# Optimization experiments

Measured on AMD Instinct MI355X. Metric: run time of the kernel, lower is better.

Reference implementation:

```python
import jax, jax.numpy as jnp
import numpy as np

NUM_CLASSES = 4
TOPK = 300            # k = min(300, A); A = 75600 >> 300
BETA = 0.1            # SmoothL1 beta
SMOOTH = 0.05         # cls label smoothing
BOX_W, OBJ_W, CLS_W = 2.0, 1.0, 1.0


def setup_inputs() -> dict:
    key = jax.random.key(0)
    k1, k2, k3 = jax.random.split(key, 3)
    predictions = jax.random.normal(k1, (32, 25200, 27), dtype=jnp.float32)
    targets_box = jax.random.uniform(k2, (32, 50, 4), dtype=jnp.float32)
    targets_cls = jax.random.randint(k3, (32, 50), 0, NUM_CLASSES, dtype=jnp.int32)
    return {"predictions": predictions, "targets_box": targets_box, "targets_cls": targets_cls}


def _xywh_to_xyxy(b):
    half_w = b[:, 2] * 0.5
    half_h = b[:, 3] * 0.5
    return jnp.stack([b[:, 0] - half_w, b[:, 1] - half_h,
                      b[:, 0] + half_w, b[:, 1] + half_h], axis=1)


def _pairwise_iou_xywh(boxes1, boxes2):
    # boxes1: [N,4], boxes2: [M,4] -> [N,M]
    b1 = _xywh_to_xyxy(boxes1)[:, None, :]   # [N,1,4]
    b2 = _xywh_to_xyxy(boxes2)[None, :, :]   # [1,M,4]
    inter_w = jnp.clip(jnp.minimum(b1[..., 2], b2[..., 2]) - jnp.maximum(b1[..., 0], b2[..., 0]), 0)
    inter_h = jnp.clip(jnp.minimum(b1[..., 3], b2[..., 3]) - jnp.maximum(b1[..., 1], b2[..., 1]), 0)
    inter = inter_w * inter_h
    area1 = (b1[..., 2] - b1[..., 0]) * (b1[..., 3] - b1[..., 1])
    area2 = (b2[..., 2] - b2[..., 0]) * (b2[..., 3] - b2[..., 1])
    union = area1 + area2 - inter
    return jnp.where(union > 0, inter / union, 0.0)


def _bce_logits(x, y):
    # BCEWithLogits: softplus(x) - x*y (numerically stable)
    return jax.nn.softplus(x) - x * y


def _smooth_l1(x, y):
    d = jnp.abs(x - y)
    return jnp.where(d < BETA, 0.5 * d * d / BETA, d - 0.5 * BETA)


def _per_sample(pred, tbox, tcls):
    # pred: [anchors, 27] -> all_anchors: [A, 9]
    nf = 5 + NUM_CLASSES
    all_anchors = pred.reshape(-1, nf)
    A = all_anchors.shape[0]
    box_logits = all_anchors[:, :4]
    obj_logits = all_anchors[:, 4]
    cls_logits = all_anchors[:, 5:5 + NUM_CLASSES]
    box_preds = jax.nn.sigmoid(box_logits)

    tcls = jnp.clip(tcls.astype(jnp.int32), 0, NUM_CLASSES - 1)   # [T]
    tboxes = jnp.clip(tbox, 0.0, 1.0)                              # [T,4]

    k = min(TOPK, A)
    _, topk_idx = jax.lax.top_k(obj_logits, k)                     # [k]
    p_boxes_k = box_preds[topk_idx]                                # [k,4]
    ious = _pairwise_iou_xywh(p_boxes_k, tboxes)                   # [k,T]
    best_idx = jnp.argmax(ious, axis=0)                            # [T]
    chosen = topk_idx[best_idx]                                    # [T]

    obj_targets = jnp.zeros((A,), pred.dtype).at[chosen].set(1.0)
    box_targets = jnp.zeros((A, 4), pred.dtype).at[chosen].set(tboxes)
    smooth_pos = 1.0 - SMOOTH
    smooth_neg = SMOOTH / max(NUM_CLASSES - 1, 1)
    cls_targets = jnp.full((A, NUM_CLASSES), smooth_neg, pred.dtype)
    cls_targets = cls_targets.at[chosen, tcls].set(smooth_pos)

    obj_weights = jnp.where(obj_targets > 0, 2.0, 0.5)
    obj_l = jnp.mean(_bce_logits(obj_logits, obj_targets) * obj_weights) * OBJ_W

    pos = (obj_targets > 0).astype(pred.dtype)                     # [A]
    npos = jnp.sum(pos)
    cls_sum = jnp.sum(_bce_logits(cls_logits, cls_targets) * pos[:, None])
    box_sum = jnp.sum(_smooth_l1(box_preds, box_targets) * pos[:, None])
    cls_l = jnp.where(npos > 0, cls_sum / (npos * NUM_CLASSES), 0.0) * CLS_W
    box_l = jnp.where(npos > 0, box_sum / (npos * 4), 0.0) * BOX_W
    return box_l, cls_l, obj_l


def reference(predictions, targets_box, targets_cls):
    box_l, cls_l, obj_l = jax.vmap(_per_sample)(predictions, targets_box, targets_cls)
    box_loss = jnp.sum(box_l)
    cls_loss = jnp.sum(cls_l)
    obj_loss = jnp.sum(obj_l)
    total_loss = box_loss + cls_loss + obj_loss
    return (total_loss, box_loss, cls_loss, obj_loss)
```

## Files before the change

### kernel.cpp

```cpp
#include <hip/hip_runtime.h>
#include <math.h>

#define NBATCH 32
#define AP     75600
#define NF     9
#define KTOP   300
#define NT     50
#define NC     4
#define APB    2048
#define UNR    8
#define NBLKA  37
#define LCAP   256
#define CCAPL  3072
#define MCAP   384
#define EQCAP  1024
#define PREFK  0xC0000000u

__device__ __forceinline__ float sp_f(float x){
    return fmaxf(x, 0.0f) + log1pf(expf(-fabsf(x)));
}
__device__ __forceinline__ float sig_f(float x){
    return 1.0f / (1.0f + expf(-x));
}
__device__ __forceinline__ unsigned fkey(float x){
    unsigned u = __float_as_uint(x);
    return (u & 0x80000000u) ? ~u : (u | 0x80000000u);
}
__device__ __forceinline__ float kinv(unsigned k){
    unsigned u = (k & 0x80000000u) ? (k & 0x7FFFFFFFu) : ~k;
    return __uint_as_float(u);
}


__global__ __launch_bounds__(256) void kA_scan(
    const float* __restrict__ pred, double* __restrict__ partials,
    unsigned* __restrict__ candKey, int* __restrict__ candIdx,
    int* __restrict__ candCnt)
{
    const int s   = blockIdx.y;
    const int blk = blockIdx.x;
    const int tid = threadIdx.x;
    __shared__ unsigned bKey[LCAP];
    __shared__ int      bIdx[LCAP];
    __shared__ int      lcnt;
    __shared__ double   wsum[4];
    if (tid == 0) lcnt = 0;
    __syncthreads();

    const float* p_s = pred + (size_t)s * (AP*NF);
    const int base = blk * APB;

    float o[UNR];
    int   j[UNR];
    bool  ok[UNR];
    #pragma unroll
    for (int u = 0; u < UNR; ++u){
        j[u]  = base + u*256 + tid;
        ok[u] = (j[u] < AP);
        o[u]  = ok[u] ? p_s[(size_t)j[u]*NF + 4] : -1.0f;
    }
    float facc = 0.0f;
    #pragma unroll
    for (int u = 0; u < UNR; ++u){
        if (ok[u]){
            facc += sp_f(o[u]);
            unsigned ky = fkey(o[u]);
            if (ky >= PREFK){
                int p = atomicAdd(&lcnt, 1);
                if (p < LCAP){ bKey[p] = ky; bIdx[p] = j[u]; }
            }
        }
    }
    double acc = (double)facc;
    for (int off = 32; off > 0; off >>= 1) acc += __shfl_down(acc, off);
    if ((tid & 63) == 0) wsum[tid >> 6] = acc;
    __syncthreads();
    if (tid == 0){
        partials[s*NBLKA + blk] = wsum[0] + wsum[1] + wsum[2] + wsum[3];
        candCnt[s*NBLKA + blk] = lcnt;
    }
    const int n = min(lcnt, LCAP);
    unsigned* gk = candKey + ((size_t)s*NBLKA + blk) * LCAP;
    int*      gi = candIdx + ((size_t)s*NBLKA + blk) * LCAP;
    for (int i = tid; i < n; i += 256){ gk[i] = bKey[i]; gi[i] = bIdx[i]; }
}

__device__ __forceinline__ void find_bin_wp(
    const unsigned* hist, int ngroups, unsigned need,
    unsigned* sGS, unsigned* sBin, unsigned* sAbove, int tid)
{
    const int wv = tid >> 6, ln = tid & 63;
    for (int g = wv; g < ngroups; g += 16){
        unsigned v = hist[g*64 + ln];
        #pragma unroll
        for (int off = 32; off > 0; off >>= 1){
            unsigned t = __shfl_down(v, off);
            if (ln + off < 64) v += t;
        }
        if (ln == 0) sGS[g] = v;
    }
    __syncthreads();
    if (wv == 0){
        unsigned gsv = (ln < ngroups) ? sGS[ln] : 0u;
        unsigned inc = gsv;
        #pragma unroll
        for (int off = 1; off < 64; off <<= 1){
            unsigned t = __shfl_down(inc, off);
            if (ln + off < 64) inc += t;
        }
        unsigned excl = inc - gsv;
        bool hit = (ln < ngroups) && (excl < need) && (need <= inc);
        unsigned long long mb = __ballot(hit);
        int gstar = __ffsll(mb) - 1;
        unsigned exG = __shfl(excl, gstar);
        unsigned y = hist[gstar*64 + ln];
        unsigned yinc = y;
        #pragma unroll
        for (int off = 1; off < 64; off <<= 1){
            unsigned t = __shfl_down(yinc, off);
            if (ln + off < 64) yinc += t;
        }
        unsigned above = exG + (yinc - y);
        bool hit2 = (above < need) && (need <= above + y);
        mb = __ballot(hit2);
        int bl = __ffsll(mb) - 1;
        unsigned ab = __shfl(above, bl);
        if (ln == 0){ *sBin = (unsigned)(gstar*64 + bl); *sAbove = ab; }
    }
    __syncthreads();
}

__global__ __launch_bounds__(1024) void kB_finish(
    const float* __restrict__ pred,
    const float* __restrict__ tboxG,
    const int*   __restrict__ tclsG,
    const unsigned* __restrict__ candKeyG, const int* __restrict__ candIdxG,
    const int* __restrict__ candCnt,
    const double* __restrict__ partials,
    float* __restrict__ lossPart)
{
    const int s   = blockIdx.x;
    const int tid = threadIdx.x;
    const int wv  = tid >> 6;
    const int ln  = tid & 63;
    const float* p_s = pred + (size_t)s * (AP*NF);

    __shared__ unsigned cKey[CCAPL];
    __shared__ int      cIdx[CCAPL];
    __shared__ unsigned hist[2048];
    __shared__ unsigned sGS[32];
    __shared__ unsigned sB1, sA1, sB2, sA2, sB3, sA3;
    __shared__ int      bOff[NBLKA + 1];
    __shared__ int      sOk;
    __shared__ int      eqList[EQCAP];
    __shared__ int      eqCnt, mCnt;
    __shared__ unsigned mKey[MCAP];
    __shared__ int      mIdx[MCAP];
    __shared__ float    mB[5][MCAP];
    __shared__ float    tXY[NT][5];
    __shared__ float    tWH[NT][4];
    __shared__ int      tCl[NT];
    __shared__ int      chosenA[NT];
    __shared__ float    corrJ[NT], clsJ[NT], boxJ[NT];
    __shared__ int      lastJ[NT];
    __shared__ double   s_spsum;

    if (tid == 0){ eqCnt = 0; mCnt = 0; }
    if (wv == 0){
        int c  = (ln < NBLKA) ? candCnt[s*NBLKA + ln] : 0;
        int of = (c > LCAP) ? 1 : 0;
        int cc = min(c, LCAP);
        int inc = cc;
        #pragma unroll
        for (int off = 1; off < 64; off <<= 1){
            int t = __shfl_up(inc, off);
            if (ln >= off) inc += t;
        }
        if (ln < NBLKA) bOff[ln + 1] = inc;
        unsigned long long anyof = __ballot(of != 0);
        if (ln == 0) bOff[0] = 0;
        if (ln == NBLKA - 1)
            sOk = (anyof == 0ull && inc >= KTOP && inc <= CCAPL) ? 1 : 0;
    }
    if (wv == 15){
        double a = (ln < NBLKA) ? partials[s*NBLKA + ln] : 0.0;
        for (int off = 32; off > 0; off >>= 1) a += __shfl_down(a, off);
        if (ln == 0) s_spsum = a;
    }
    __syncthreads();
    const bool fast = (sOk != 0);
    const int  n    = fast ? bOff[NBLKA] : 0;

    if (fast){
        for (int b = wv; b < NBLKA; b += 16){
            const int c = min(candCnt[s*NBLKA + b], LCAP);
            const int o = bOff[b];
            const unsigned* gk = candKeyG + ((size_t)s*NBLKA + b) * LCAP;
            const int*      gi = candIdxG + ((size_t)s*NBLKA + b) * LCAP;
            for (int i = ln; i < c; i += 64){ cKey[o+i] = gk[i]; cIdx[o+i] = gi[i]; }
        }
    }
    for (int i = tid; i < 2048; i += 1024) hist[i] = 0;
    __syncthreads();
    if (fast){
        for (int i = tid; i < n; i += 1024) atomicAdd(&hist[cKey[i] >> 21], 1u);
    } else {
        for (int i = tid; i < AP; i += 1024)
            atomicAdd(&hist[fkey(p_s[(size_t)i*NF + 4]) >> 21], 1u);
    }
    __syncthreads();
    find_bin_wp(hist, 32, KTOP, sGS, &sB1, &sA1, tid);
    const unsigned b1 = sB1, ab1 = sA1;
    const unsigned need2 = KTOP - ab1;

    for (int i = tid; i < 2048; i += 1024) hist[i] = 0;
    __syncthreads();
    if (fast){
        for (int i = tid; i < n; i += 1024){
            unsigned ky = cKey[i];
            if ((ky >> 21) == b1) atomicAdd(&hist[(ky >> 10) & 0x7FFu], 1u);
        }
    } else {
        for (int i = tid; i < AP; i += 1024){
            unsigned ky = fkey(p_s[(size_t)i*NF + 4]);
            if ((ky >> 21) == b1) atomicAdd(&hist[(ky >> 10) & 0x7FFu], 1u);
        }
    }
    __syncthreads();
    find_bin_wp(hist, 32, need2, sGS, &sB2, &sA2, tid);
    const unsigned b2 = sB2, ab2 = sA2;
    const unsigned need3 = need2 - ab2;
    const unsigned pref  = (b1 << 11) | b2;

    if (tid < 1024) hist[tid] = 0;
    __syncthreads();
    if (fast){
        for (int i = tid; i < n; i += 1024){
            unsigned ky = cKey[i];
            if ((ky >> 10) == pref) atomicAdd(&hist[ky & 0x3FFu], 1u);
        }
    } else {
        for (int i = tid; i < AP; i += 1024){
            unsigned ky = fkey(p_s[(size_t)i*NF + 4]);
            if ((ky >> 10) == pref) atomicAdd(&hist[ky & 0x3FFu], 1u);
        }
    }
    __syncthreads();
    find_bin_wp(hist, 16, need3, sGS, &sB3, &sA3, tid);
    const unsigned b3 = sB3, ab3 = sA3;
    const unsigned needEq = need3 - ab3;
    const unsigned T = (b1 << 21) | (b2 << 10) | b3;

    if (fast){
        for (int i = tid; i < n; i += 1024){
            if (cKey[i] == T){
                int p = atomicAdd(&eqCnt, 1);
                if (p < EQCAP) eqList[p] = cIdx[i];
            }
        }
    } else {
        for (int i = tid; i < AP; i += 1024){
            if (fkey(p_s[(size_t)i*NF + 4]) == T){
                int p = atomicAdd(&eqCnt, 1);
                if (p < EQCAP) eqList[p] = i;
            }
        }
    }
    __syncthreads();
    const int ne = min(eqCnt, EQCAP);

    const int dom = fast ? n : AP;
    for (int base = wv*64; base < dom; base += 1024){
        int i = base + ln;
        bool mflag = false; unsigned ky = 0; int ix = 0;
        if (i < dom){
            if (fast){ ky = cKey[i]; ix = cIdx[i]; }
            else     { ky = fkey(p_s[(size_t)i*NF + 4]); ix = i; }
            if (ky > T) mflag = true;
            else if (ky == T){
                int r = 0;
                for (int j = 0; j < ne; ++j) r += (eqList[j] < ix) ? 1 : 0;
                mflag = ((unsigned)r < needEq);
            }
        }
        unsigned long long msk = __ballot(mflag);
        int bpos = 0;
        if (ln == 0 && msk) bpos = atomicAdd(&mCnt, (int)__popcll(msk));
        bpos = __shfl(bpos, 0);
        if (mflag){
            int pos = bpos + (int)__popcll(msk & ((1ull << ln) - 1ull));
            if (pos < MCAP){ mKey[pos] = ky; mIdx[pos] = ix; }
        }
    }
    __syncthreads();
    const int kM = min(mCnt, MCAP);

    for (int m = tid; m < kM; m += 1024){
        const float* row = p_s + (size_t)mIdx[m] * NF;
        float bx = sig_f(row[0]), by = sig_f(row[1]);
        float bw = sig_f(row[2]), bh = sig_f(row[3]);
        float hw = bw * 0.5f, hh = bh * 0.5f;
        float x1 = bx - hw, y1 = by - hh, x2 = bx + hw, y2 = by + hh;
        mB[0][m] = x1; mB[1][m] = y1; mB[2][m] = x2; mB[3][m] = y2;
        mB[4][m] = (x2 - x1) * (y2 - y1);
    }
    if (tid >= 512 && tid < 512 + NT){
        int t = tid - 512;
        const float* tb = tboxG + ((size_t)s * NT + t) * 4;
        float cx = fminf(fmaxf(tb[0], 0.f), 1.f);
        float cy = fminf(fmaxf(tb[1], 0.f), 1.f);
        float w  = fminf(fmaxf(tb[2], 0.f), 1.f);
        float h  = fminf(fmaxf(tb[3], 0.f), 1.f);
        tWH[t][0] = cx; tWH[t][1] = cy; tWH[t][2] = w; tWH[t][3] = h;
        float hw = w * 0.5f, hh = h * 0.5f;
        float x1 = cx - hw, y1 = cy - hh, x2 = cx + hw, y2 = cy + hh;
        tXY[t][0] = x1; tXY[t][1] = y1; tXY[t][2] = x2; tXY[t][3] = y2;
        tXY[t][4] = (x2 - x1) * (y2 - y1);
        int c = tclsG[(size_t)s * NT + t];
        tCl[t] = min(max(c, 0), NC - 1);
    }
    __syncthreads();

    for (int t = wv; t < NT; t += 16){
        float tx1 = tXY[t][0], ty1 = tXY[t][1], tx2 = tXY[t][2], ty2 = tXY[t][3];
        float ta  = tXY[t][4];
        float    bIou = -1.0f; unsigned bKy = 0; int bIx = 0x7FFFFFFF;
        for (int m = ln; m < kM; m += 64){
            float iw = fminf(mB[2][m], tx2) - fmaxf(mB[0][m], tx1);
            iw = fmaxf(iw, 0.0f);
            float ih = fminf(mB[3][m], ty2) - fmaxf(mB[1][m], ty1);
            ih = fmaxf(ih, 0.0f);
            float inter = iw * ih;
            float uni = mB[4][m] + ta - inter;
            float iou = (uni > 0.0f) ? (inter / uni) : 0.0f;
            unsigned ky = mKey[m]; int ix = mIdx[m];
            if (iou > bIou || (iou == bIou && (ky > bKy || (ky == bKy && ix < bIx)))){
                bIou = iou; bKy = ky; bIx = ix;
            }
        }
        #pragma unroll
        for (int off = 32; off > 0; off >>= 1){
            float    oI = __shfl_down(bIou, off);
            unsigned oK = __shfl_down(bKy,  off);
            int      oX = __shfl_down(bIx,  off);
            bool take = (ln + off < 64) &&
                        (oI > bIou || (oI == bIou && (oK > bKy || (oK == bKy && oX < bIx))));
            if (take){ bIou = oI; bKy = oK; bIx = oX; }
        }
        if (ln == 0) chosenA[t] = bIx;
    }
    __syncthreads();

    if (tid < NT){
        int a = chosenA[tid];
        bool last = true;
        for (int j2 = tid + 1; j2 < NT; ++j2) if (chosenA[j2] == a) last = false;
        float corr = 0.f, clsv = 0.f, boxv = 0.f;
        if (last){
            const float* row = p_s + (size_t)a * NF;
            float o = row[4];
            float spo = sp_f(o);
            corr = 2.0f * (spo - o) - 0.5f * spo;
            unsigned mask = 0;
            for (int j2 = 0; j2 < NT; ++j2)
                if (chosenA[j2] == a) mask |= (1u << tCl[j2]);
            const float smooth_neg = (float)(0.05 / 3.0);
            for (int c = 0; c < NC; ++c){
                float x = row[5 + c];
                float t = ((mask >> c) & 1u) ? 0.95f : smooth_neg;
                clsv += sp_f(x) - x * t;
            }
            for (int c = 0; c < 4; ++c){
                float p = sig_f(row[c]);
                float d = fabsf(p - tWH[tid][c]);
                boxv += (d < 0.1f) ? (0.5f * d * d / 0.1f) : (d - 0.05f);
            }
        }
        lastJ[tid] = last ? 1 : 0;
        corrJ[tid] = corr; clsJ[tid] = clsv; boxJ[tid] = boxv;
    }
    __syncthreads();

    if (tid == 0){
        double corrS = 0, clsS = 0, boxS = 0; int np = 0;
        for (int j = 0; j < NT; ++j){
            if (lastJ[j]){ np++; corrS += corrJ[j]; clsS += clsJ[j]; boxS += boxJ[j]; }
        }
        float obj_l = (float)((0.5 * s_spsum + corrS) / (double)AP);
        float cls_l = (np > 0) ? (float)(clsS / ((double)np * NC)) : 0.f;
        float box_l = (np > 0) ? (float)(boxS / ((double)np * 4) * 2.0) : 0.f;
        lossPart[s*4 + 0] = box_l;
        lossPart[s*4 + 1] = cls_l;
        lossPart[s*4 + 2] = obj_l;
    }
}

__global__ void k5_reduce(const float* __restrict__ lossPart, float* __restrict__ out){
    if (threadIdx.x == 0){
        double b = 0, c = 0, o = 0;
        for (int s2 = 0; s2 < NBATCH; ++s2){
            b += (double)lossPart[s2*4 + 0];
            c += (double)lossPart[s2*4 + 1];
            o += (double)lossPart[s2*4 + 2];
        }
        out[1] = (float)b; out[2] = (float)c; out[3] = (float)o;
        out[0] = (float)(b + c + o);
    }
}


__device__ __forceinline__ unsigned load_key(const unsigned* k_s, const float* p_s, int i){
    return k_s ? k_s[i] : fkey(p_s[i*NF + 4]);
}

__global__ void build_keys_kernel(const float* __restrict__ pred, unsigned* __restrict__ keys){
    int s = blockIdx.y;
    int a = blockIdx.x * 256 + threadIdx.x;
    if (a < AP){
        float o = pred[(size_t)s * (AP*NF) + (size_t)a * NF + 4];
        keys[s * AP + a] = fkey(o);
    }
}

__device__ void find_bin(unsigned* hist, unsigned* ssup, int* sbin, unsigned* sabove,
                         unsigned need, int tid){
    if (tid < 32){
        unsigned a2 = 0;
        for (int i = 0; i < 64; ++i) a2 += hist[tid*64 + i];
        ssup[tid] = a2;
    }
    __syncthreads();
    if (tid == 0){
        unsigned a2 = 0; int g = 31;
        for (; g > 0; --g){ if (a2 + ssup[g] >= need) break; a2 += ssup[g]; }
        int b = g*64 + 63;
        for (;;){ unsigned h = hist[b]; if (a2 + h >= need || b == g*64) break; a2 += h; --b; }
        *sbin = b; *sabove = a2;
    }
    __syncthreads();
}

__global__ __launch_bounds__(1024) void loss_kernel_full(
    const float* __restrict__ pred,
    const unsigned* __restrict__ keysG,
    const float* __restrict__ tboxG,
    const int*   __restrict__ tclsG,
    float* __restrict__ out)
{
    const int s   = blockIdx.x;
    const int tid = threadIdx.x;
    const float*    p_s = pred + (size_t)s * (AP*NF);
    const unsigned* k_s = keysG ? (keysG + s * AP) : nullptr;

    __shared__ unsigned hist[2048];
    __shared__ unsigned ssup[32];
    __shared__ int sbin; __shared__ unsigned sabove;
    __shared__ double wsum[16];
    __shared__ double s_spsum;
    __shared__ unsigned tkKey[KTOP]; __shared__ int tkIdx[KTOP];
    __shared__ int eqIdx[2048];
    __shared__ int nGt, nEq;
    __shared__ int sIdx[KTOP];
    __shared__ float cand[KTOP][5];
    __shared__ float tXY[NT][5];
    __shared__ float tWH[NT][4];
    __shared__ int   tCl[NT];
    __shared__ int   chosenA[NT];
    __shared__ float corrJ[NT], clsJ[NT], boxJ[NT];
    __shared__ int   lastJ[NT];

    for (int i = tid; i < 2048; i += 1024) hist[i] = 0;
    if (tid == 0){ nGt = 0; nEq = 0; }
    __syncthreads();
    double acc = 0.0;
    for (int i = tid; i < AP; i += 1024){
        unsigned ky = load_key(k_s, p_s, i);
        atomicAdd(&hist[ky >> 21], 1u);
        acc += (double)sp_f(kinv(ky));
    }
    for (int off = 32; off > 0; off >>= 1) acc += __shfl_down(acc, off);
    if ((tid & 63) == 0) wsum[tid >> 6] = acc;
    __syncthreads();
    if (tid == 0){
        double t = 0.0;
        for (int w = 0; w < 16; ++w) t += wsum[w];
        s_spsum = t;
    }
    __syncthreads();

    find_bin(hist, ssup, &sbin, &sabove, KTOP, tid);
    const int b1 = sbin; const unsigned above1 = sabove;
    const unsigned need2 = KTOP - above1;
    __syncthreads();

    for (int i = tid; i < 2048; i += 1024) hist[i] = 0;
    __syncthreads();
    for (int i = tid; i < AP; i += 1024){
        unsigned ky = load_key(k_s, p_s, i);
        if ((int)(ky >> 21) == b1) atomicAdd(&hist[(ky >> 10) & 0x7FFu], 1u);
    }
    __syncthreads();
    find_bin(hist, ssup, &sbin, &sabove, need2, tid);
    const int b2 = sbin; const unsigned above2 = sabove;
    const unsigned need3 = need2 - above2;
    const unsigned pref  = ((unsigned)b1 << 11) | (unsigned)b2;
    __syncthreads();

    for (int i = tid; i < 2048; i += 1024) hist[i] = 0;
    __syncthreads();
    for (int i = tid; i < AP; i += 1024){
        unsigned ky = load_key(k_s, p_s, i);
        if ((ky >> 10) == pref) atomicAdd(&hist[ky & 0x3FFu], 1u);
    }
    __syncthreads();
    find_bin(hist, ssup, &sbin, &sabove, need3, tid);
    const int b3 = sbin; const unsigned above3 = sabove;
    const unsigned needEq = need3 - above3;
    const unsigned T      = ((unsigned)b1 << 21) | ((unsigned)b2 << 10) | (unsigned)b3;
    const unsigned cntGt  = above1 + above2 + above3;
    __syncthreads();

    for (int i = tid; i < AP; i += 1024){
        unsigned ky = load_key(k_s, p_s, i);
        if (ky > T){
            int p = atomicAdd(&nGt, 1);
            if (p < KTOP){ tkKey[p] = ky; tkIdx[p] = i; }
        } else if (ky == T){
            int p = atomicAdd(&nEq, 1);
            if (p < 2048) eqIdx[p] = i;
        }
    }
    __syncthreads();
    {
        int ne = min(nEq, 2048);
        for (int t = tid; t < ne; t += 1024){
            int mine = eqIdx[t]; int r = 0;
            for (int j = 0; j < ne; ++j) r += (eqIdx[j] < mine) ? 1 : 0;
            if ((unsigned)r < needEq){
                int p = (int)cntGt + r;
                if (p < KTOP){ tkKey[p] = T; tkIdx[p] = mine; }
            }
        }
    }
    __syncthreads();

    if (tid < KTOP){
        unsigned myk = tkKey[tid]; int myi = tkIdx[tid];
        int r = 0;
        for (int j = 0; j < KTOP; ++j){
            unsigned kj = tkKey[j]; int ij = tkIdx[j];
            r += (kj > myk || (kj == myk && ij < myi)) ? 1 : 0;
        }
        sIdx[r] = myi;
    }
    __syncthreads();

    if (tid < KTOP){
        int a = sIdx[tid];
        const float* row = p_s + a * NF;
        float bx = sig_f(row[0]), by = sig_f(row[1]);
        float bw = sig_f(row[2]), bh = sig_f(row[3]);
        float hw = bw * 0.5f, hh = bh * 0.5f;
        float x1 = bx - hw, y1 = by - hh, x2 = bx + hw, y2 = by + hh;
        cand[tid][0] = x1; cand[tid][1] = y1; cand[tid][2] = x2; cand[tid][3] = y2;
        cand[tid][4] = (x2 - x1) * (y2 - y1);
    }
    if (tid < NT){
        const float* tb = tboxG + ((size_t)s * NT + tid) * 4;
        float cx = fminf(fmaxf(tb[0], 0.f), 1.f);
        float cy = fminf(fmaxf(tb[1], 0.f), 1.f);
        float w  = fminf(fmaxf(tb[2], 0.f), 1.f);
        float h  = fminf(fmaxf(tb[3], 0.f), 1.f);
        tWH[tid][0] = cx; tWH[tid][1] = cy; tWH[tid][2] = w; tWH[tid][3] = h;
        float hw = w * 0.5f, hh = h * 0.5f;
        float x1 = cx - hw, y1 = cy - hh, x2 = cx + hw, y2 = cy + hh;
        tXY[tid][0] = x1; tXY[tid][1] = y1; tXY[tid][2] = x2; tXY[tid][3] = y2;
        tXY[tid][4] = (x2 - x1) * (y2 - y1);
        int c = tclsG[(size_t)s * NT + tid];
        tCl[tid] = min(max(c, 0), NC - 1);
    }
    __syncthreads();

    if (tid < NT){
        float tx1 = tXY[tid][0], ty1 = tXY[tid][1], tx2 = tXY[tid][2], ty2 = tXY[tid][3];
        float ta  = tXY[tid][4];
        float best = -1.0f; int bi = 0;
        for (int i = 0; i < KTOP; ++i){
            float iw = fminf(cand[i][2], tx2) - fmaxf(cand[i][0], tx1);
            iw = fmaxf(iw, 0.0f);
            float ih = fminf(cand[i][3], ty2) - fmaxf(cand[i][1], ty1);
            ih = fmaxf(ih, 0.0f);
            float inter = iw * ih;
            float uni = cand[i][4] + ta - inter;
            float iou = (uni > 0.0f) ? (inter / uni) : 0.0f;
            if (iou > best){ best = iou; bi = i; }
        }
        chosenA[tid] = sIdx[bi];
    }
    __syncthreads();

    if (tid < NT){
        int a = chosenA[tid];
        bool last = true;
        for (int j2 = tid + 1; j2 < NT; ++j2) if (chosenA[j2] == a) last = false;
        float corr = 0.f, clsv = 0.f, boxv = 0.f;
        if (last){
            const float* row = p_s + a * NF;
            float o = row[4];
            float spo = sp_f(o);
            corr = 2.0f * (spo - o) - 0.5f * spo;
            unsigned mask = 0;
            for (int j2 = 0; j2 < NT; ++j2)
                if (chosenA[j2] == a) mask |= (1u << tCl[j2]);
            const float smooth_neg = (float)(0.05 / 3.0);
            for (int c = 0; c < NC; ++c){
                float x = row[5 + c];
                float t = ((mask >> c) & 1u) ? 0.95f : smooth_neg;
                clsv += sp_f(x) - x * t;
            }
            for (int c = 0; c < 4; ++c){
                float p = sig_f(row[c]);
                float d = fabsf(p - tWH[tid][c]);
                boxv += (d < 0.1f) ? (0.5f * d * d / 0.1f) : (d - 0.05f);
            }
        }
        lastJ[tid] = last ? 1 : 0;
        corrJ[tid] = corr; clsJ[tid] = clsv; boxJ[tid] = boxv;
    }
    __syncthreads();

    if (tid == 0){
        double corrS = 0, clsS = 0, boxS = 0; int np = 0;
        for (int j = 0; j < NT; ++j){
            if (lastJ[j]){ np++; corrS += corrJ[j]; clsS += clsJ[j]; boxS += boxJ[j]; }
        }
        float obj_l = (float)((0.5 * s_spsum + corrS) / (double)AP);
        float cls_l = (np > 0) ? (float)(clsS / ((double)np * NC)) : 0.f;
        float box_l = (np > 0) ? (float)(boxS / ((double)np * 4) * 2.0) : 0.f;
        atomicAdd(&out[1], box_l);
        atomicAdd(&out[2], cls_l);
        atomicAdd(&out[3], obj_l);
        atomicAdd(&out[0], box_l + cls_l + obj_l);
    }
}


static inline size_t align256(size_t x){ return (x + 255) & ~(size_t)255; }

extern "C" void kernel_launch(void* const* d_in, const int* in_sizes, int n_in,
                              void* d_out, int out_size, void* d_ws, size_t ws_size,
                              hipStream_t stream) {
    const float* pred = (const float*)d_in[0];
    const float* tbox = (const float*)d_in[1];
    const int*   tcls = (const int*)d_in[2];
    float* out = (float*)d_out;

    const size_t oCnt   = 0;
    const size_t oPart  = align256(oCnt + (size_t)NBATCH * NBLKA * sizeof(int));
    const size_t oCKey  = align256(oPart + (size_t)NBATCH * NBLKA * sizeof(double));
    const size_t oCIdx  = align256(oCKey + (size_t)NBATCH * NBLKA * LCAP * sizeof(unsigned));
    const size_t oLoss  = align256(oCIdx + (size_t)NBATCH * NBLKA * LCAP * sizeof(int));
    const size_t need   = oLoss + (size_t)NBATCH * 4 * sizeof(float);
    const size_t keysB  = (size_t)NBATCH * AP * sizeof(unsigned);

    if (ws_size >= need){
        char* ws = (char*)d_ws;
        int*      candCnt = (int*)     (ws + oCnt);
        double*   parts   = (double*)  (ws + oPart);
        unsigned* candKey = (unsigned*)(ws + oCKey);
        int*      candIdx = (int*)     (ws + oCIdx);
        float*    lossP   = (float*)   (ws + oLoss);

        dim3 gwA(NBLKA, NBATCH);
        kA_scan<<<gwA, 256, 0, stream>>>(pred, parts, candKey, candIdx, candCnt);
        kB_finish<<<NBATCH, 1024, 0, stream>>>(pred, tbox, tcls, candKey, candIdx,
                                               candCnt, parts, lossP);
        k5_reduce<<<1, 64, 0, stream>>>(lossP, out);
    } else {
        hipMemsetAsync(d_out, 0, (size_t)out_size * sizeof(float), stream);
        unsigned* keys = (ws_size >= keysB) ? (unsigned*)d_ws : nullptr;
        if (keys){
            dim3 grid((AP + 255) / 256, NBATCH);
            build_keys_kernel<<<grid, 256, 0, stream>>>(pred, keys);
        }
        loss_kernel_full<<<NBATCH, 1024, 0, stream>>>(pred, keys, tbox, tcls, out);
    }
}
```

Measured before the change: 52.75 us.

## Split objectness scan into one-element-per-thread blocks with multi-chunk prefix

The scan kernel now has each 256-thread block handle 256 anchors instead of 2048, raising the block count per sample from 37 to 296 and shrinking the per-block candidate buffer to 64. The second kernel's prefix sum over block candidate counts and its softplus partial reduction now loop over 64-wide chunks with a carry. The aim is more parallelism and latency hiding for the strided objectness loads in the first pass. The cost is more partials and candidate slots to read and combine in the consumer, more launch blocks, and a higher chance that a block exceeds its 64-slot cap and forces the slow path.

```diff
diff --git a/kernel.cpp b/kernel.cpp
--- a/kernel.cpp
+++ b/kernel.cpp
@@ -7,10 +7,8 @@
 #define KTOP   300
 #define NT     50
 #define NC     4
-#define APB    2048
-#define UNR    8
-#define NBLKA  37
-#define LCAP   256
+#define NBLKA  296
+#define LCAP   64
 #define CCAPL  3072
 #define MCAP   384
 #define EQCAP  1024
@@ -48,27 +46,15 @@
     __syncthreads();
 
     const float* p_s = pred + (size_t)s * (AP*NF);
-    const int base = blk * APB;
-
-    float o[UNR];
-    int   j[UNR];
-    bool  ok[UNR];
-    #pragma unroll
-    for (int u = 0; u < UNR; ++u){
-        j[u]  = base + u*256 + tid;
-        ok[u] = (j[u] < AP);
-        o[u]  = ok[u] ? p_s[(size_t)j[u]*NF + 4] : -1.0f;
-    }
-    float facc = 0.0f;
-    #pragma unroll
-    for (int u = 0; u < UNR; ++u){
-        if (ok[u]){
-            facc += sp_f(o[u]);
-            unsigned ky = fkey(o[u]);
-            if (ky >= PREFK){
-                int p = atomicAdd(&lcnt, 1);
-                if (p < LCAP){ bKey[p] = ky; bIdx[p] = j[u]; }
-            }
+    const int a = blk*256 + tid;
+    const bool ok = (a < AP);
+    float o = ok ? p_s[(size_t)a*NF + 4] : -1.0f;
+    float facc = ok ? sp_f(o) : 0.0f;
+    if (ok){
+        unsigned ky = fkey(o);
+        if (ky >= PREFK){
+            int p = atomicAdd(&lcnt, 1);
+            if (p < LCAP){ bKey[p] = ky; bIdx[p] = a; }
         }
     }
     double acc = (double)facc;
@@ -167,24 +153,34 @@
 
     if (tid == 0){ eqCnt = 0; mCnt = 0; }
     if (wv == 0){
-        int c  = (ln < NBLKA) ? candCnt[s*NBLKA + ln] : 0;
-        int of = (c > LCAP) ? 1 : 0;
-        int cc = min(c, LCAP);
-        int inc = cc;
-        #pragma unroll
-        for (int off = 1; off < 64; off <<= 1){
-            int t = __shfl_up(inc, off);
-            if (ln >= off) inc += t;
-        }
-        if (ln < NBLKA) bOff[ln + 1] = inc;
-        unsigned long long anyof = __ballot(of != 0);
-        if (ln == 0) bOff[0] = 0;
-        if (ln == NBLKA - 1)
-            sOk = (anyof == 0ull && inc >= KTOP && inc <= CCAPL) ? 1 : 0;
+        int carry = 0; int anyof = 0;
+        for (int base = 0; base < NBLKA; base += 64){
+            int b   = base + ln;
+            int raw = (b < NBLKA) ? candCnt[s*NBLKA + b] : 0;
+            anyof  |= (raw > LCAP) ? 1 : 0;
+            int inc = min(raw, LCAP);
+            #pragma unroll
+            for (int off = 1; off < 64; off <<= 1){
+                int t = __shfl_up(inc, off);
+                if (ln >= off) inc += t;
+            }
+            if (b < NBLKA) bOff[b + 1] = carry + inc;
+            carry += __shfl(inc, 63);
+        }
+        unsigned long long m = __ballot(anyof != 0);
+        if (ln == 0){
+            bOff[0] = 0;
+            sOk = (m == 0ull && carry >= KTOP && carry <= CCAPL) ? 1 : 0;
+        }
     }
     if (wv == 15){
-        double a = (ln < NBLKA) ? partials[s*NBLKA + ln] : 0.0;
-        for (int off = 32; off > 0; off >>= 1) a += __shfl_down(a, off);
+        double a = 0.0;
+        for (int base = 0; base < NBLKA; base += 64){
+            int b = base + ln;
+            double v = (b < NBLKA) ? partials[s*NBLKA + b] : 0.0;
+            for (int off = 32; off > 0; off >>= 1) v += __shfl_down(v, off);
+            if (ln == 0) a += v;
+        }
         if (ln == 0) s_spsum = a;
     }
     __syncthreads();
```

New measurement: 60.28 us. +14.3%, slower.

## Fuse final reduction into finish kernel via atomic ticket; grid-stride scan

Applied to the files above, without the earlier changes.

Removes the separate single-thread reduce kernel by having the last-finishing block of kB_finish (picked with an atomic ticket counter reset in kA_scan) sum the per-sample losses and write the output. The scan kernel moves from an 8-way unrolled fixed chunk to a grid-stride loop over 40 blocks, accumulating in double, and the per-block candidate cap doubles to 512. This saves one kernel launch and its gap, but the grid-stride loop gives up the batched independent loads, and the double-precision per-element accumulation may add cost.

```diff
diff --git a/kernel.cpp b/kernel.cpp
--- a/kernel.cpp
+++ b/kernel.cpp
@@ -7,10 +7,8 @@
 #define KTOP   300
 #define NT     50
 #define NC     4
-#define APB    2048
-#define UNR    8
-#define NBLKA  37
-#define LCAP   256
+#define NBLKA  40
+#define LCAP   512
 #define CCAPL  3072
 #define MCAP   384
 #define EQCAP  1024
@@ -35,7 +33,7 @@
 __global__ __launch_bounds__(256) void kA_scan(
     const float* __restrict__ pred, double* __restrict__ partials,
     unsigned* __restrict__ candKey, int* __restrict__ candIdx,
-    int* __restrict__ candCnt)
+    int* __restrict__ candCnt, unsigned* __restrict__ ticket)
 {
     const int s   = blockIdx.y;
     const int blk = blockIdx.x;
@@ -45,33 +43,20 @@
     __shared__ int      lcnt;
     __shared__ double   wsum[4];
     if (tid == 0) lcnt = 0;
+    if (s == 0 && blk == 0 && tid == 1) *ticket = 0u;
     __syncthreads();
 
     const float* p_s = pred + (size_t)s * (AP*NF);
-    const int base = blk * APB;
-
-    float o[UNR];
-    int   j[UNR];
-    bool  ok[UNR];
-    #pragma unroll
-    for (int u = 0; u < UNR; ++u){
-        j[u]  = base + u*256 + tid;
-        ok[u] = (j[u] < AP);
-        o[u]  = ok[u] ? p_s[(size_t)j[u]*NF + 4] : -1.0f;
-    }
-    float facc = 0.0f;
-    #pragma unroll
-    for (int u = 0; u < UNR; ++u){
-        if (ok[u]){
-            facc += sp_f(o[u]);
-            unsigned ky = fkey(o[u]);
-            if (ky >= PREFK){
-                int p = atomicAdd(&lcnt, 1);
-                if (p < LCAP){ bKey[p] = ky; bIdx[p] = j[u]; }
-            }
-        }
-    }
-    double acc = (double)facc;
+    double acc = 0.0;
+    for (int i = blk*256 + tid; i < AP; i += NBLKA*256){
+        float o = p_s[(size_t)i*NF + 4];
+        acc += (double)sp_f(o);
+        unsigned ky = fkey(o);
+        if (ky >= PREFK){
+            int p = atomicAdd(&lcnt, 1);
+            if (p < LCAP){ bKey[p] = ky; bIdx[p] = i; }
+        }
+    }
     for (int off = 32; off > 0; off >>= 1) acc += __shfl_down(acc, off);
     if ((tid & 63) == 0) wsum[tid >> 6] = acc;
     __syncthreads();
@@ -137,7 +122,8 @@
     const unsigned* __restrict__ candKeyG, const int* __restrict__ candIdxG,
     const int* __restrict__ candCnt,
     const double* __restrict__ partials,
-    float* __restrict__ lossPart)
+    float* __restrict__ lossPart, unsigned* __restrict__ ticket,
+    float* __restrict__ out)
 {
     const int s   = blockIdx.x;
     const int tid = threadIdx.x;
@@ -164,6 +150,7 @@
     __shared__ float    corrJ[NT], clsJ[NT], boxJ[NT];
     __shared__ int      lastJ[NT];
     __shared__ double   s_spsum;
+    __shared__ int      sTicket;
 
     if (tid == 0){ eqCnt = 0; mCnt = 0; }
     if (wv == 0){
@@ -393,15 +380,21 @@
         lossPart[s*4 + 1] = cls_l;
         lossPart[s*4 + 2] = obj_l;
     }
-}
-
-__global__ void k5_reduce(const float* __restrict__ lossPart, float* __restrict__ out){
-    if (threadIdx.x == 0){
+    __syncthreads();
+
+    if (tid == 0){
+        __threadfence();
+        sTicket = (int)atomicAdd(ticket, 1u);
+    }
+    __syncthreads();
+    if (sTicket == NBATCH - 1 && tid == 0){
+        __threadfence();
+        volatile const float* lp = lossPart;
         double b = 0, c = 0, o = 0;
         for (int s2 = 0; s2 < NBATCH; ++s2){
-            b += (double)lossPart[s2*4 + 0];
-            c += (double)lossPart[s2*4 + 1];
-            o += (double)lossPart[s2*4 + 2];
+            b += (double)lp[s2*4 + 0];
+            c += (double)lp[s2*4 + 1];
+            o += (double)lp[s2*4 + 2];
         }
         out[1] = (float)b; out[2] = (float)c; out[3] = (float)o;
         out[0] = (float)(b + c + o);
@@ -660,7 +653,8 @@
     const size_t oCKey  = align256(oPart + (size_t)NBATCH * NBLKA * sizeof(double));
     const size_t oCIdx  = align256(oCKey + (size_t)NBATCH * NBLKA * LCAP * sizeof(unsigned));
     const size_t oLoss  = align256(oCIdx + (size_t)NBATCH * NBLKA * LCAP * sizeof(int));
-    const size_t need   = oLoss + (size_t)NBATCH * 4 * sizeof(float);
+    const size_t oTick  = align256(oLoss + (size_t)NBATCH * 4 * sizeof(float));
+    const size_t need   = oTick + 256;
     const size_t keysB  = (size_t)NBATCH * AP * sizeof(unsigned);
 
     if (ws_size >= need){
@@ -670,12 +664,12 @@
         unsigned* candKey = (unsigned*)(ws + oCKey);
         int*      candIdx = (int*)     (ws + oCIdx);
         float*    lossP   = (float*)   (ws + oLoss);
+        unsigned* ticket  = (unsigned*)(ws + oTick);
 
         dim3 gwA(NBLKA, NBATCH);
-        kA_scan<<<gwA, 256, 0, stream>>>(pred, parts, candKey, candIdx, candCnt);
+        kA_scan<<<gwA, 256, 0, stream>>>(pred, parts, candKey, candIdx, candCnt, ticket);
         kB_finish<<<NBATCH, 1024, 0, stream>>>(pred, tbox, tcls, candKey, candIdx,
-                                               candCnt, parts, lossP);
-        k5_reduce<<<1, 64, 0, stream>>>(lossP, out);
+                                               candCnt, parts, lossP, ticket, out);
     } else {
         hipMemsetAsync(d_out, 0, (size_t)out_size * sizeof(float), stream);
         unsigned* keys = (ws_size >= keysB) ? (unsigned*)d_ws : nullptr;
```

Result: slower. 57.88 us (+9.7%).
